# Performance work log

Measured on AMD Instinct MI355X. Metric: run time of the kernel, lower is better.

## Reference

```python
import jax, jax.numpy as jnp
import numpy as np

NUM_HEADS = 8
HEAD_DIM = 64
EMBED = NUM_HEADS * HEAD_DIM  # 512


def setup_inputs() -> dict:
    key = jax.random.key(0)
    ks = jax.random.split(key, 8)
    B, S = 4, 2048
    s = 1.0 / np.sqrt(HEAD_DIM)
    so = 1.0 / np.sqrt(EMBED)
    return {
        "queries": jax.random.normal(ks[0], (B, S, EMBED), jnp.float32),
        "keys": jax.random.normal(ks[1], (B, S, EMBED), jnp.float32),
        "values": jax.random.normal(ks[2], (B, S, EMBED), jnp.float32),
        "Wq": jax.random.uniform(ks[3], (HEAD_DIM, HEAD_DIM), jnp.float32, -s, s),
        "Wk": jax.random.uniform(ks[4], (HEAD_DIM, HEAD_DIM), jnp.float32, -s, s),
        "Wv": jax.random.uniform(ks[5], (HEAD_DIM, HEAD_DIM), jnp.float32, -s, s),
        "Wo": jax.random.uniform(ks[6], (EMBED, EMBED), jnp.float32, -so, so),
        "bo": jax.random.uniform(ks[7], (EMBED,), jnp.float32, -so, so),
    }


def reference(queries, keys, values, Wq, Wk, Wv, Wo, bo):
    B, Sq, _ = queries.shape
    # Faithful to source: keys/values are (buggily) reshaped from `queries`;
    # with equal seq lens this means k/v come from the queries tensor.
    q = queries.reshape(B, Sq, NUM_HEADS, HEAD_DIM)
    k = q
    v = q
    # per-head linear: torch Linear(x) = x @ W.T
    q = jnp.einsum('bshd,ed->bshe', q, Wq)
    k = jnp.einsum('bshd,ed->bshe', k, Wk)
    v = jnp.einsum('bshd,ed->bshe', v, Wv)
    sim = jnp.einsum('bqhd,bkhd->bhqk', q, k)  # [B,H,Sq,Sk]
    attn = jax.nn.softmax(sim * (1.0 / np.sqrt(HEAD_DIM)), axis=-1)
    out = jnp.einsum('bhqk,bkhd->bqhd', attn, v)
    out = out.reshape(B, Sq, EMBED)
    return out @ Wo.T + bo
```

## Files before the change

kernel.cpp:

```cpp
#include <hip/hip_runtime.h>
#include <cstddef>

#define S_ 2048
#define E_ 512
#define SPLIT_STRIDE 4194304u

typedef __attribute__((ext_vector_type(8)))  short bf16x8;
typedef __attribute__((ext_vector_type(16))) float f32x16;

__device__ __forceinline__ unsigned short f2bf(float f) {
    union { float f; unsigned u; } v; v.f = f;
    return (unsigned short)((v.u + 0x7FFFu + ((v.u >> 16) & 1u)) >> 16);
}
__device__ __forceinline__ unsigned pk2bf(float a, float b) {
    union { float f; unsigned u; } x, y; x.f = a; y.f = b;
    return __builtin_amdgcn_perm(y.u + 0x8000u, x.u + 0x8000u, 0x07060302u);
}
__device__ __forceinline__ float bflo(unsigned u) {
    union { unsigned u; float f; } v; v.u = u << 16; return v.f;
}
__device__ __forceinline__ float bfhi(unsigned u) {
    union { unsigned u; float f; } v; v.u = u & 0xffff0000u; return v.f;
}
__device__ __forceinline__ float fexp2(float x) {
    float r;
    asm("v_exp_f32 %0, %1" : "=v"(r) : "v"(x));
    return r;
}

__global__ __launch_bounds__(256) void prep_all(const float* __restrict__ X,
                                                const float* __restrict__ Wq,
                                                const float* __restrict__ Wk,
                                                const float* __restrict__ Wo,
                                                const float* __restrict__ Wv,
                                                unsigned short* __restrict__ Xbf,
                                                unsigned short* __restrict__ XTg,
                                                unsigned short* __restrict__ GT,
                                                unsigned short* __restrict__ W2) {
    __shared__ unsigned Tt[2320];
    const int bi = blockIdx.x, tid = threadIdx.x;
    if (bi < 1024) {
        const int st = bi & 31, h = (bi >> 5) & 7, b = bi >> 8;
        const int s0 = st * 64;
        const int j = tid >> 2, g = tid & 3;
        const float* src = X + ((size_t)(b * S_ + s0 + j) * E_) + h * 64 + g * 16;
        unsigned short us[16];
#pragma unroll
        for (int i = 0; i < 16; i += 4) {
            float4 f = *(const float4*)(src + i);
            us[i] = f2bf(f.x); us[i + 1] = f2bf(f.y);
            us[i + 2] = f2bf(f.z); us[i + 3] = f2bf(f.w);
        }
        size_t xb = ((size_t)(b * S_ + s0 + j) * E_) + h * 64 + g * 16;
        *(uint4*)&Xbf[xb]     = *(uint4*)&us[0];
        *(uint4*)&Xbf[xb + 8] = *(uint4*)&us[8];
        {
            const unsigned* p = (const unsigned*)us;
            const int base = (j >> 4) * 580 + (j & 15) * 36 + g * 8;
            *(uint4*)&Tt[base]     = *(const uint4*)&p[0];
            *(uint4*)&Tt[base + 4] = *(const uint4*)&p[4];
        }
        __syncthreads();
        const int d = tid >> 2;
        const int pm[16] = {0,1,2,3,8,9,10,11,4,5,6,7,12,13,14,15};
        const unsigned sel = (d & 1) ? 0x07060302u : 0x05040100u;
        const int rb = g * 580;
        const int d2 = d >> 1;
        unsigned o32[8];
#pragma unroll
        for (int k = 0; k < 8; ++k) {
            unsigned va = Tt[rb + pm[2 * k]     * 36 + d2];
            unsigned vb = Tt[rb + (pm[2 * k] + 1) * 36 + d2];
            o32[k] = __builtin_amdgcn_perm(vb, va, sel);
        }
        size_t tb = ((size_t)((b * 8 + h) * 64 + d)) * S_ + s0 + g * 16;
        *(uint4*)&XTg[tb]     = *(const uint4*)&o32[0];
        *(uint4*)&XTg[tb + 8] = *(const uint4*)&o32[4];
    } else if (bi < 1040) {
        int idx = (bi - 1024) * 256 + tid;
        int c = idx >> 6, d = idx & 63;
        float acc = 0.f;
#pragma unroll 8
        for (int e = 0; e < 64; ++e) acc += Wq[e * 64 + d] * Wk[e * 64 + c];
        GT[c * 64 + d] = f2bf(acc * 0.18033688011112042f);
    } else {
        int idx = (bi - 1040) * 256 + tid;
        int e = idx >> 9, f = idx & 511;
        int h = f >> 6, c = f & 63;
        const float* wo = Wo + e * 512 + h * 64;
        float acc = 0.f;
#pragma unroll 8
        for (int d = 0; d < 64; ++d) acc += wo[d] * Wv[d * 64 + c];
        W2[idx] = f2bf(acc);
    }
}

__global__ __launch_bounds__(128, 2) void attn_mfma(const unsigned short* __restrict__ Xbf,
                                                    const unsigned short* __restrict__ XTg,
                                                    const unsigned short* __restrict__ GT,
                                                    unsigned short* __restrict__ AOp,
                                                    float* __restrict__ Lp) {
    __shared__ union SM {
        unsigned short Q[128][72];
        unsigned char  cb[2][2][8192];
        unsigned short AOt[128][72];
    } sm;

    const int tid = threadIdx.x;
    const int w = tid >> 6, lane = tid & 63;
    const int lm = lane & 31, lh = lane >> 5;
    const int h = blockIdx.x & 7;
    const int rest = blockIdx.x >> 3;
    const int qt = rest & 15, b = (rest >> 4) & 3, split = rest >> 6;
    const int s0 = qt * 128, sk0 = split * (S_ / 2);

    {
        const int r = tid >> 1, c = (tid & 1) * 32;
#pragma unroll
        for (int p = 0; p < 2; ++p) {
            const unsigned short* src = Xbf + ((size_t)(b * S_ + s0 + 64 * p + r)) * E_ + h * 64 + c;
#pragma unroll
            for (int u = 0; u < 4; ++u)
                *(uint4*)&sm.Q[64 * p + r][c + u * 8] = *(const uint4*)(src + u * 8);
        }
    }
    __syncthreads();

    bf16x8 Ufrag[2][4];
    {
        f32x16 ua[2][2];
#pragma unroll
        for (int mt = 0; mt < 2; ++mt)
#pragma unroll
            for (int nt = 0; nt < 2; ++nt)
#pragma unroll
                for (int i = 0; i < 16; ++i) ua[mt][nt][i] = 0.f;
#pragma unroll
        for (int ks = 0; ks < 4; ++ks) {
            bf16x8 bG0 = *(const bf16x8*)&GT[(lm +  0) * 64 + ks * 16 + lh * 8];
            bf16x8 bG1 = *(const bf16x8*)&GT[(lm + 32) * 64 + ks * 16 + lh * 8];
#pragma unroll
            for (int mt = 0; mt < 2; ++mt) {
                bf16x8 aQ = *(const bf16x8*)&sm.Q[64 * w + 32 * mt + lm][ks * 16 + lh * 8];
                ua[mt][0] = __builtin_amdgcn_mfma_f32_32x32x16_bf16(aQ, bG0, ua[mt][0], 0, 0, 0);
                ua[mt][1] = __builtin_amdgcn_mfma_f32_32x32x16_bf16(aQ, bG1, ua[mt][1], 0, 0, 0);
            }
        }
#pragma unroll
        for (int mt = 0; mt < 2; ++mt)
#pragma unroll
            for (int nt = 0; nt < 2; ++nt)
#pragma unroll
                for (int r = 0; r < 16; ++r)
                    sm.Q[64 * w + 32 * mt + (r & 3) + 8 * (r >> 2) + 4 * lh][lm + 32 * nt] =
                        f2bf(ua[mt][nt][r]);
#pragma unroll
        for (int g = 0; g < 2; ++g)
#pragma unroll
            for (int ks = 0; ks < 4; ++ks)
                Ufrag[g][ks] = *(const bf16x8*)&sm.Q[64 * w + 32 * g + lm][ks * 16 + lh * 8];
    }
    __syncthreads();

    const int il = lane >> 3;
    const int swc = ((lane & 7) ^ (il & 7)) * 8;
    const unsigned short* gX0 = Xbf + ((size_t)(b * S_ + sk0 + 32 * w + il)) * E_ + h * 64 + swc;
    const unsigned short* gT0 = XTg + ((size_t)((b * 8 + h) * 64 + 32 * w + il)) * S_ + sk0 + swc;

#pragma unroll
    for (int i8 = 0; i8 < 4; ++i8) {
        __builtin_amdgcn_global_load_lds((const unsigned*)(gX0 + (size_t)i8 * 8 * E_),
                                         (unsigned*)&sm.cb[0][0][(4 * w + i8) * 1024], 16, 0, 0);
        __builtin_amdgcn_global_load_lds((const unsigned*)(gT0 + (size_t)i8 * 8 * S_),
                                         (unsigned*)&sm.cb[0][1][(4 * w + i8) * 1024], 16, 0, 0);
    }
    __syncthreads();

    float lsum0 = 0.f, lsum1 = 0.f;
    f32x16 AO[2][2];
#pragma unroll
    for (int mt = 0; mt < 2; ++mt)
#pragma unroll
        for (int nt = 0; nt < 2; ++nt)
#pragma unroll
            for (int i = 0; i < 16; ++i) AO[mt][nt][i] = 0.f;

    f32x16 zv;
#pragma unroll
    for (int i = 0; i < 16; ++i) zv[i] = 0.f;

    const int xorr = (lm & 7) << 4;

    for (int ck = 0; ck < 16; ++ck) {
        const int rb = ck & 1;
        if (ck < 15) {
            const unsigned short* sX = gX0 + (size_t)(ck + 1) * 64 * E_;
            const unsigned short* sT = gT0 + (ck + 1) * 64;
            unsigned char* dX = &sm.cb[rb ^ 1][0][4 * w * 1024];
            unsigned char* dT = &sm.cb[rb ^ 1][1][4 * w * 1024];
#pragma unroll
            for (int i8 = 0; i8 < 4; ++i8) {
                __builtin_amdgcn_global_load_lds((const unsigned*)(sX + (size_t)i8 * 8 * E_),
                                                 (unsigned*)(dX + i8 * 1024), 16, 0, 0);
                __builtin_amdgcn_global_load_lds((const unsigned*)(sT + (size_t)i8 * 8 * S_),
                                                 (unsigned*)(dT + i8 * 1024), 16, 0, 0);
            }
        }

        const unsigned char* bX = sm.cb[rb][0];
        const unsigned char* bT = sm.cb[rb][1];

        f32x16 sc[2][2];
        __builtin_amdgcn_s_setprio(1);
#pragma unroll
        for (int mt = 0; mt < 2; ++mt) {
            bf16x8 aX = *(const bf16x8*)(bX + (32 * mt + lm) * 128 + ((lh * 16) ^ xorr));
            sc[mt][0] = __builtin_amdgcn_mfma_f32_32x32x16_bf16(aX, Ufrag[0][0], zv, 0, 0, 0);
            sc[mt][1] = __builtin_amdgcn_mfma_f32_32x32x16_bf16(aX, Ufrag[1][0], zv, 0, 0, 0);
        }
#pragma unroll
        for (int ks = 1; ks < 4; ++ks)
#pragma unroll
            for (int mt = 0; mt < 2; ++mt) {
                bf16x8 aX = *(const bf16x8*)(bX + (32 * mt + lm) * 128 + ((ks * 32 + lh * 16) ^ xorr));
                sc[mt][0] = __builtin_amdgcn_mfma_f32_32x32x16_bf16(aX, Ufrag[0][ks], sc[mt][0], 0, 0, 0);
                sc[mt][1] = __builtin_amdgcn_mfma_f32_32x32x16_bf16(aX, Ufrag[1][ks], sc[mt][1], 0, 0, 0);
            }
        __builtin_amdgcn_s_setprio(0);

#pragma unroll
        for (int js = 0; js < 4; ++js) {
            const int mt = js >> 1, jh = js & 1;
            union { unsigned u[4]; bf16x8 v; } bP0, bP1;
#pragma unroll
            for (int i = 0; i < 4; ++i) {
                const int qq = 2 * jh + (i >> 1);
                float pa = fexp2(sc[mt][0][qq * 4 + 2 * (i & 1)]);
                float pb = fexp2(sc[mt][0][qq * 4 + 2 * (i & 1) + 1]);
                lsum0 += pa + pb;
                bP0.u[i] = pk2bf(pa, pb);
                float pc = fexp2(sc[mt][1][qq * 4 + 2 * (i & 1)]);
                float pd = fexp2(sc[mt][1][qq * 4 + 2 * (i & 1) + 1]);
                lsum1 += pc + pd;
                bP1.u[i] = pk2bf(pc, pd);
            }
            __builtin_amdgcn_s_setprio(1);
#pragma unroll
            for (int mtv = 0; mtv < 2; ++mtv) {
                bf16x8 aT = *(const bf16x8*)(bT + (32 * mtv + lm) * 128 + ((js * 32 + lh * 16) ^ xorr));
                AO[mtv][0] = __builtin_amdgcn_mfma_f32_32x32x16_bf16(aT, bP0.v, AO[mtv][0], 0, 0, 0);
                AO[mtv][1] = __builtin_amdgcn_mfma_f32_32x32x16_bf16(aT, bP1.v, AO[mtv][1], 0, 0, 0);
            }
            __builtin_amdgcn_s_setprio(0);
        }
        __syncthreads();
    }

    lsum0 += __shfl_xor(lsum0, 32);
    lsum1 += __shfl_xor(lsum1, 32);
#pragma unroll
    for (int mtv = 0; mtv < 2; ++mtv)
#pragma unroll
        for (int nt = 0; nt < 2; ++nt)
#pragma unroll
            for (int qq = 0; qq < 4; ++qq) {
                const int d0 = 32 * mtv + 8 * qq + 4 * lh;
                const int row = 64 * w + 32 * nt + lm;
                *(unsigned*)&sm.AOt[row][d0] =
                    pk2bf(AO[mtv][nt][qq * 4 + 0], AO[mtv][nt][qq * 4 + 1]);
                *(unsigned*)&sm.AOt[row][d0 + 2] =
                    pk2bf(AO[mtv][nt][qq * 4 + 2], AO[mtv][nt][qq * 4 + 3]);
            }
    __syncthreads();
    {
        const int r = tid >> 1, c = (tid & 1) * 32;
#pragma unroll
        for (int p = 0; p < 2; ++p) {
            unsigned short* dst = AOp + (size_t)split * SPLIT_STRIDE
                                + ((size_t)(b * S_ + s0 + 64 * p + r)) * E_ + h * 64 + c;
#pragma unroll
            for (int u = 0; u < 4; ++u)
                *(uint4*)(dst + u * 8) = *(const uint4*)&sm.AOt[64 * p + r][c + u * 8];
        }
    }
    if (lane < 32) {
        const size_t lb = ((size_t)(split * 4 + b) * 8 + h) * S_ + s0 + 64 * w;
        Lp[lb + lm]      = lsum0;
        Lp[lb + 32 + lm] = lsum1;
    }
}

__global__ __launch_bounds__(256) void out_gemm_bf(const unsigned short* __restrict__ AOp,
                                                   const float* __restrict__ Lp,
                                                   const unsigned short* __restrict__ W2,
                                                   const float* __restrict__ bo,
                                                   float* __restrict__ out) {
    __shared__ unsigned short At[64][72];
    __shared__ unsigned short Bt[64][72];
    const int tid = threadIdx.x;
    const int w = tid >> 6, lane = tid & 63;
    const int lm = lane & 31, lh = lane >> 5;
    const int et = blockIdx.x >> 7;
    const int rt = (blockIdx.x & 7) * 16 + ((blockIdx.x >> 3) & 15);
    const int r0 = rt * 64, e0 = et * 64;
    const int rr = tid >> 2, cc = (tid & 3) * 16;
    const int srow = r0 + rr, bb = srow >> 11, ss = srow & 2047;

    f32x16 acc;
#pragma unroll
    for (int i = 0; i < 16; ++i) acc[i] = 0.f;

    for (int k0 = 0; k0 < 512; k0 += 64) {
        const int hh = k0 >> 6;
        const float linv = 1.0f / (Lp[((size_t)(bb)*8 + hh) * S_ + ss] +
                                   Lp[((size_t)(4 + bb) * 8 + hh) * S_ + ss]);
        __syncthreads();
        {
            const unsigned short* a0 = AOp + (size_t)srow * 512 + k0 + cc;
            const unsigned short* a1 = a0 + SPLIT_STRIDE;
            uint4 u0 = *(const uint4*)a0, u0b = *(const uint4*)(a0 + 8);
            uint4 u1 = *(const uint4*)a1, u1b = *(const uint4*)(a1 + 8);
            uint4 o, ob;
            o.x  = pk2bf((bflo(u0.x) + bflo(u1.x)) * linv, (bfhi(u0.x) + bfhi(u1.x)) * linv);
            o.y  = pk2bf((bflo(u0.y) + bflo(u1.y)) * linv, (bfhi(u0.y) + bfhi(u1.y)) * linv);
            o.z  = pk2bf((bflo(u0.z) + bflo(u1.z)) * linv, (bfhi(u0.z) + bfhi(u1.z)) * linv);
            o.w  = pk2bf((bflo(u0.w) + bflo(u1.w)) * linv, (bfhi(u0.w) + bfhi(u1.w)) * linv);
            ob.x = pk2bf((bflo(u0b.x) + bflo(u1b.x)) * linv, (bfhi(u0b.x) + bfhi(u1b.x)) * linv);
            ob.y = pk2bf((bflo(u0b.y) + bflo(u1b.y)) * linv, (bfhi(u0b.y) + bfhi(u1b.y)) * linv);
            ob.z = pk2bf((bflo(u0b.z) + bflo(u1b.z)) * linv, (bfhi(u0b.z) + bfhi(u1b.z)) * linv);
            ob.w = pk2bf((bflo(u0b.w) + bflo(u1b.w)) * linv, (bfhi(u0b.w) + bfhi(u1b.w)) * linv);
            *(uint4*)&At[rr][cc]     = o;
            *(uint4*)&At[rr][cc + 8] = ob;
            const unsigned short* sb = W2 + (size_t)(e0 + rr) * 512 + k0 + cc;
            *(uint4*)&Bt[rr][cc]     = *(const uint4*)sb;
            *(uint4*)&Bt[rr][cc + 8] = *(const uint4*)(sb + 8);
        }
        __syncthreads();
#pragma unroll
        for (int ks = 0; ks < 4; ++ks) {
            bf16x8 aA = *(const bf16x8*)&At[32 * (w & 1) + lm][ks * 16 + lh * 8];
            bf16x8 bW = *(const bf16x8*)&Bt[32 * (w >> 1) + lm][ks * 16 + lh * 8];
            acc = __builtin_amdgcn_mfma_f32_32x32x16_bf16(aA, bW, acc, 0, 0, 0);
        }
    }
    const float bv = bo[e0 + 32 * (w >> 1) + lm];
#pragma unroll
    for (int r = 0; r < 16; ++r) {
        int orow = r0 + 32 * (w & 1) + (r & 3) + 8 * (r >> 2) + 4 * lh;
        out[(size_t)orow * 512 + e0 + 32 * (w >> 1) + lm] = acc[r] + bv;
    }
}

extern "C" void kernel_launch(void* const* d_in, const int* in_sizes, int n_in,
                              void* d_out, int out_size, void* d_ws, size_t ws_size,
                              hipStream_t stream) {
    (void)in_sizes; (void)n_in; (void)out_size; (void)ws_size;
    const float* X  = (const float*)d_in[0];
    const float* Wq = (const float*)d_in[3];
    const float* Wk = (const float*)d_in[4];
    const float* Wv = (const float*)d_in[5];
    const float* Wo = (const float*)d_in[6];
    const float* bo = (const float*)d_in[7];

    float* ws = (float*)d_ws;
    unsigned short* W2bf = (unsigned short*)ws;
    unsigned short* GT   = (unsigned short*)(ws + 131072);
    unsigned short* Xbf  = (unsigned short*)(ws + 133120);
    unsigned short* XTg  = (unsigned short*)(ws + 2230272);
    unsigned short* AOp  = (unsigned short*)(ws + 4327424);
    float*          Lp   = ws + 8521728;

    prep_all   <<<2064, 256, 0, stream>>>(X, Wq, Wk, Wo, Wv, Xbf, XTg, GT, W2bf);
    attn_mfma  <<<1024, 128, 0, stream>>>(Xbf, XTg, GT, AOp, Lp);
    out_gemm_bf<<<1024, 256, 0, stream>>>(AOp, Lp, W2bf, bo, (float*)d_out);
}
```

Baseline: 161.1 us.

## Split attention key range four ways with smaller KV chunks

Templates the attention and output GEMM kernels on the number of key splits. When the workspace is large enough it launches 2048 attention blocks, each covering a quarter of the keys, and the output GEMM sums four partial outputs and row sums. KV chunks shrink from 64 to 32 keys, which halves the LDS buffers and allows a launch bound of 4 blocks per SM for more parallelism and occupancy. The cost is more partial-output traffic and reduction work in the output GEMM, plus more loop iterations and barriers per key.

```diff
diff --git a/kernel.cpp b/kernel.cpp
--- a/kernel.cpp
+++ b/kernel.cpp
@@ -95,14 +95,17 @@
     }
 }
 
-__global__ __launch_bounds__(128, 2) void attn_mfma(const unsigned short* __restrict__ Xbf,
+template<int NSPLIT>
+__global__ __launch_bounds__(128, 4) void attn_mfma(const unsigned short* __restrict__ Xbf,
                                                     const unsigned short* __restrict__ XTg,
                                                     const unsigned short* __restrict__ GT,
                                                     unsigned short* __restrict__ AOp,
                                                     float* __restrict__ Lp) {
+    constexpr int KPB = S_ / NSPLIT;
+    constexpr int CHUNKS = KPB / 32;
     __shared__ union SM {
         unsigned short Q[128][72];
-        unsigned char  cb[2][2][8192];
+        unsigned char  cb[2][2][4096];
         unsigned short AOt[128][72];
     } sm;
 
@@ -112,7 +115,7 @@
     const int h = blockIdx.x & 7;
     const int rest = blockIdx.x >> 3;
     const int qt = rest & 15, b = (rest >> 4) & 3, split = rest >> 6;
-    const int s0 = qt * 128, sk0 = split * (S_ / 2);
+    const int s0 = qt * 128, sk0 = split * KPB;
 
     {
         const int r = tid >> 1, c = (tid & 1) * 32;
@@ -162,47 +165,50 @@
     }
     __syncthreads();
 
-    const int il = lane >> 3;
-    const int swc = ((lane & 7) ^ (il & 7)) * 8;
-    const unsigned short* gX0 = Xbf + ((size_t)(b * S_ + sk0 + 32 * w + il)) * E_ + h * 64 + swc;
-    const unsigned short* gT0 = XTg + ((size_t)((b * 8 + h) * 64 + 32 * w + il)) * S_ + sk0 + swc;
-
-#pragma unroll
-    for (int i8 = 0; i8 < 4; ++i8) {
+    const unsigned short* gX0 = Xbf
+        + ((size_t)(b * S_ + sk0 + 16 * w + (lane >> 3))) * E_ + h * 64
+        + ((lane & 7) ^ (lane >> 3)) * 8;
+    const unsigned short* gT0 = XTg
+        + ((size_t)((b * 8 + h) * 64 + 32 * w + (lane >> 2))) * S_ + sk0
+        + ((lane & 3) ^ ((lane >> 2) & 3)) * 8;
+
+#pragma unroll
+    for (int i8 = 0; i8 < 2; ++i8) {
         __builtin_amdgcn_global_load_lds((const unsigned*)(gX0 + (size_t)i8 * 8 * E_),
-                                         (unsigned*)&sm.cb[0][0][(4 * w + i8) * 1024], 16, 0, 0);
-        __builtin_amdgcn_global_load_lds((const unsigned*)(gT0 + (size_t)i8 * 8 * S_),
-                                         (unsigned*)&sm.cb[0][1][(4 * w + i8) * 1024], 16, 0, 0);
+                                         (unsigned*)&sm.cb[0][0][w * 2048 + i8 * 1024], 16, 0, 0);
+        __builtin_amdgcn_global_load_lds((const unsigned*)(gT0 + (size_t)i8 * 16 * S_),
+                                         (unsigned*)&sm.cb[0][1][w * 2048 + i8 * 1024], 16, 0, 0);
     }
     __syncthreads();
 
     float lsum0 = 0.f, lsum1 = 0.f;
     f32x16 AO[2][2];
 #pragma unroll
-    for (int mt = 0; mt < 2; ++mt)
-#pragma unroll
-        for (int nt = 0; nt < 2; ++nt)
-#pragma unroll
-            for (int i = 0; i < 16; ++i) AO[mt][nt][i] = 0.f;
+    for (int mtv = 0; mtv < 2; ++mtv)
+#pragma unroll
+        for (int g = 0; g < 2; ++g)
+#pragma unroll
+            for (int i = 0; i < 16; ++i) AO[mtv][g][i] = 0.f;
 
     f32x16 zv;
 #pragma unroll
     for (int i = 0; i < 16; ++i) zv[i] = 0.f;
 
-    const int xorr = (lm & 7) << 4;
-
-    for (int ck = 0; ck < 16; ++ck) {
+    const int xorrX = (lm & 7) << 4;
+    const int xorrT = (lm & 3) << 4;
+
+    for (int ck = 0; ck < CHUNKS; ++ck) {
         const int rb = ck & 1;
-        if (ck < 15) {
-            const unsigned short* sX = gX0 + (size_t)(ck + 1) * 64 * E_;
-            const unsigned short* sT = gT0 + (ck + 1) * 64;
-            unsigned char* dX = &sm.cb[rb ^ 1][0][4 * w * 1024];
-            unsigned char* dT = &sm.cb[rb ^ 1][1][4 * w * 1024];
-#pragma unroll
-            for (int i8 = 0; i8 < 4; ++i8) {
+        if (ck < CHUNKS - 1) {
+            const unsigned short* sX = gX0 + (size_t)(ck + 1) * 32 * E_;
+            const unsigned short* sT = gT0 + (ck + 1) * 32;
+            unsigned char* dX = &sm.cb[rb ^ 1][0][w * 2048];
+            unsigned char* dT = &sm.cb[rb ^ 1][1][w * 2048];
+#pragma unroll
+            for (int i8 = 0; i8 < 2; ++i8) {
                 __builtin_amdgcn_global_load_lds((const unsigned*)(sX + (size_t)i8 * 8 * E_),
                                                  (unsigned*)(dX + i8 * 1024), 16, 0, 0);
-                __builtin_amdgcn_global_load_lds((const unsigned*)(sT + (size_t)i8 * 8 * S_),
+                __builtin_amdgcn_global_load_lds((const unsigned*)(sT + (size_t)i8 * 16 * S_),
                                                  (unsigned*)(dT + i8 * 1024), 16, 0, 0);
             }
         }
@@ -210,44 +216,40 @@
         const unsigned char* bX = sm.cb[rb][0];
         const unsigned char* bT = sm.cb[rb][1];
 
-        f32x16 sc[2][2];
+        f32x16 sc[2];
         __builtin_amdgcn_s_setprio(1);
-#pragma unroll
-        for (int mt = 0; mt < 2; ++mt) {
-            bf16x8 aX = *(const bf16x8*)(bX + (32 * mt + lm) * 128 + ((lh * 16) ^ xorr));
-            sc[mt][0] = __builtin_amdgcn_mfma_f32_32x32x16_bf16(aX, Ufrag[0][0], zv, 0, 0, 0);
-            sc[mt][1] = __builtin_amdgcn_mfma_f32_32x32x16_bf16(aX, Ufrag[1][0], zv, 0, 0, 0);
-        }
-#pragma unroll
-        for (int ks = 1; ks < 4; ++ks)
-#pragma unroll
-            for (int mt = 0; mt < 2; ++mt) {
-                bf16x8 aX = *(const bf16x8*)(bX + (32 * mt + lm) * 128 + ((ks * 32 + lh * 16) ^ xorr));
-                sc[mt][0] = __builtin_amdgcn_mfma_f32_32x32x16_bf16(aX, Ufrag[0][ks], sc[mt][0], 0, 0, 0);
-                sc[mt][1] = __builtin_amdgcn_mfma_f32_32x32x16_bf16(aX, Ufrag[1][ks], sc[mt][1], 0, 0, 0);
-            }
+        {
+            bf16x8 aX = *(const bf16x8*)(bX + lm * 128 + ((lh * 16) ^ xorrX));
+            sc[0] = __builtin_amdgcn_mfma_f32_32x32x16_bf16(aX, Ufrag[0][0], zv, 0, 0, 0);
+            sc[1] = __builtin_amdgcn_mfma_f32_32x32x16_bf16(aX, Ufrag[1][0], zv, 0, 0, 0);
+        }
+#pragma unroll
+        for (int ks = 1; ks < 4; ++ks) {
+            bf16x8 aX = *(const bf16x8*)(bX + lm * 128 + ((ks * 32 + lh * 16) ^ xorrX));
+            sc[0] = __builtin_amdgcn_mfma_f32_32x32x16_bf16(aX, Ufrag[0][ks], sc[0], 0, 0, 0);
+            sc[1] = __builtin_amdgcn_mfma_f32_32x32x16_bf16(aX, Ufrag[1][ks], sc[1], 0, 0, 0);
+        }
         __builtin_amdgcn_s_setprio(0);
 
 #pragma unroll
-        for (int js = 0; js < 4; ++js) {
-            const int mt = js >> 1, jh = js & 1;
+        for (int s = 0; s < 2; ++s) {
             union { unsigned u[4]; bf16x8 v; } bP0, bP1;
 #pragma unroll
             for (int i = 0; i < 4; ++i) {
-                const int qq = 2 * jh + (i >> 1);
-                float pa = fexp2(sc[mt][0][qq * 4 + 2 * (i & 1)]);
-                float pb = fexp2(sc[mt][0][qq * 4 + 2 * (i & 1) + 1]);
+                const int ra = 8 * s + 4 * (i >> 1) + 2 * (i & 1);
+                float pa = fexp2(sc[0][ra]);
+                float pb = fexp2(sc[0][ra + 1]);
                 lsum0 += pa + pb;
                 bP0.u[i] = pk2bf(pa, pb);
-                float pc = fexp2(sc[mt][1][qq * 4 + 2 * (i & 1)]);
-                float pd = fexp2(sc[mt][1][qq * 4 + 2 * (i & 1) + 1]);
+                float pc = fexp2(sc[1][ra]);
+                float pd = fexp2(sc[1][ra + 1]);
                 lsum1 += pc + pd;
                 bP1.u[i] = pk2bf(pc, pd);
             }
             __builtin_amdgcn_s_setprio(1);
 #pragma unroll
             for (int mtv = 0; mtv < 2; ++mtv) {
-                bf16x8 aT = *(const bf16x8*)(bT + (32 * mtv + lm) * 128 + ((js * 32 + lh * 16) ^ xorr));
+                bf16x8 aT = *(const bf16x8*)(bT + (32 * mtv + lm) * 64 + ((s * 32 + lh * 16) ^ xorrT));
                 AO[mtv][0] = __builtin_amdgcn_mfma_f32_32x32x16_bf16(aT, bP0.v, AO[mtv][0], 0, 0, 0);
                 AO[mtv][1] = __builtin_amdgcn_mfma_f32_32x32x16_bf16(aT, bP1.v, AO[mtv][1], 0, 0, 0);
             }
@@ -290,6 +292,7 @@
     }
 }
 
+template<int NSPLIT>
 __global__ __launch_bounds__(256) void out_gemm_bf(const unsigned short* __restrict__ AOp,
                                                    const float* __restrict__ Lp,
                                                    const unsigned short* __restrict__ W2,
@@ -312,23 +315,39 @@
 
     for (int k0 = 0; k0 < 512; k0 += 64) {
         const int hh = k0 >> 6;
-        const float linv = 1.0f / (Lp[((size_t)(bb)*8 + hh) * S_ + ss] +
-                                   Lp[((size_t)(4 + bb) * 8 + hh) * S_ + ss]);
+        float lt = 0.f;
+#pragma unroll
+        for (int sp = 0; sp < NSPLIT; ++sp)
+            lt += Lp[((size_t)(sp * 4 + bb) * 8 + hh) * S_ + ss];
+        const float linv = 1.0f / lt;
         __syncthreads();
         {
             const unsigned short* a0 = AOp + (size_t)srow * 512 + k0 + cc;
-            const unsigned short* a1 = a0 + SPLIT_STRIDE;
-            uint4 u0 = *(const uint4*)a0, u0b = *(const uint4*)(a0 + 8);
-            uint4 u1 = *(const uint4*)a1, u1b = *(const uint4*)(a1 + 8);
+            float fa[16];
+#pragma unroll
+            for (int i = 0; i < 16; ++i) fa[i] = 0.f;
+#pragma unroll
+            for (int sp = 0; sp < NSPLIT; ++sp) {
+                const unsigned short* ap = a0 + (size_t)sp * SPLIT_STRIDE;
+                uint4 ua = *(const uint4*)ap, ub = *(const uint4*)(ap + 8);
+                const unsigned* pu = (const unsigned*)&ua;
+                const unsigned* pv = (const unsigned*)&ub;
+#pragma unroll
+                for (int k = 0; k < 4; ++k) {
+                    fa[2 * k]     += bflo(pu[k]);
+                    fa[2 * k + 1] += bfhi(pu[k]);
+                    fa[8 + 2 * k]     += bflo(pv[k]);
+                    fa[8 + 2 * k + 1] += bfhi(pv[k]);
+                }
+            }
             uint4 o, ob;
-            o.x  = pk2bf((bflo(u0.x) + bflo(u1.x)) * linv, (bfhi(u0.x) + bfhi(u1.x)) * linv);
-            o.y  = pk2bf((bflo(u0.y) + bflo(u1.y)) * linv, (bfhi(u0.y) + bfhi(u1.y)) * linv);
-            o.z  = pk2bf((bflo(u0.z) + bflo(u1.z)) * linv, (bfhi(u0.z) + bfhi(u1.z)) * linv);
-            o.w  = pk2bf((bflo(u0.w) + bflo(u1.w)) * linv, (bfhi(u0.w) + bfhi(u1.w)) * linv);
-            ob.x = pk2bf((bflo(u0b.x) + bflo(u1b.x)) * linv, (bfhi(u0b.x) + bfhi(u1b.x)) * linv);
-            ob.y = pk2bf((bflo(u0b.y) + bflo(u1b.y)) * linv, (bfhi(u0b.y) + bfhi(u1b.y)) * linv);
-            ob.z = pk2bf((bflo(u0b.z) + bflo(u1b.z)) * linv, (bfhi(u0b.z) + bfhi(u1b.z)) * linv);
-            ob.w = pk2bf((bflo(u0b.w) + bflo(u1b.w)) * linv, (bfhi(u0b.w) + bfhi(u1b.w)) * linv);
+            unsigned* po  = (unsigned*)&o;
+            unsigned* pob = (unsigned*)&ob;
+#pragma unroll
+            for (int k = 0; k < 4; ++k) {
+                po[k]  = pk2bf(fa[2 * k] * linv, fa[2 * k + 1] * linv);
+                pob[k] = pk2bf(fa[8 + 2 * k] * linv, fa[8 + 2 * k + 1] * linv);
+            }
             *(uint4*)&At[rr][cc]     = o;
             *(uint4*)&At[rr][cc + 8] = ob;
             const unsigned short* sb = W2 + (size_t)(e0 + rr) * 512 + k0 + cc;
@@ -354,7 +373,7 @@
 extern "C" void kernel_launch(void* const* d_in, const int* in_sizes, int n_in,
                               void* d_out, int out_size, void* d_ws, size_t ws_size,
                               hipStream_t stream) {
-    (void)in_sizes; (void)n_in; (void)out_size; (void)ws_size;
+    (void)in_sizes; (void)n_in; (void)out_size;
     const float* X  = (const float*)d_in[0];
     const float* Wq = (const float*)d_in[3];
     const float* Wk = (const float*)d_in[4];
@@ -368,9 +387,17 @@
     unsigned short* Xbf  = (unsigned short*)(ws + 133120);
     unsigned short* XTg  = (unsigned short*)(ws + 2230272);
     unsigned short* AOp  = (unsigned short*)(ws + 4327424);
-    float*          Lp   = ws + 8521728;
-
-    prep_all   <<<2064, 256, 0, stream>>>(X, Wq, Wk, Wo, Wv, Xbf, XTg, GT, W2bf);
-    attn_mfma  <<<1024, 128, 0, stream>>>(Xbf, XTg, GT, AOp, Lp);
-    out_gemm_bf<<<1024, 256, 0, stream>>>(AOp, Lp, W2bf, bo, (float*)d_out);
-}
+
+    prep_all<<<2064, 256, 0, stream>>>(X, Wq, Wk, Wo, Wv, Xbf, XTg, GT, W2bf);
+
+    const size_t need4 = (size_t)(12716032 + 262144) * 4;
+    if (ws_size >= need4) {
+        float* Lp = ws + 12716032;
+        attn_mfma<4><<<2048, 128, 0, stream>>>(Xbf, XTg, GT, AOp, Lp);
+        out_gemm_bf<4><<<1024, 256, 0, stream>>>(AOp, Lp, W2bf, bo, (float*)d_out);
+    } else {
+        float* Lp = ws + 8521728;
+        attn_mfma<2><<<1024, 128, 0, stream>>>(Xbf, XTg, GT, AOp, Lp);
+        out_gemm_bf<2><<<1024, 256, 0, stream>>>(AOp, Lp, W2bf, bo, (float*)d_out);
+    }
+}
```

New measurement: 227.3 us. 1.41x slower.

## Load K/V MFMA fragments directly from global memory instead of LDS staging

Applied to the files above, without the earlier changes.

Removes the double-buffered LDS staging of K and V tiles, which used async global_load_lds and a barrier per chunk. Each wave now reads its MFMA operand fragments straight from global memory (relying on L1/L2 caches), which drops per-iteration __syncthreads and shrinks shared memory to allow more residency. The trade-off is uncoalesced 16-byte global reads, duplicated across the two waves in a block, with no prefetch overlap, so load latency sits directly on the MFMA path.

```diff
diff --git a/kernel.cpp b/kernel.cpp
--- a/kernel.cpp
+++ b/kernel.cpp
@@ -102,7 +102,6 @@
                                                     float* __restrict__ Lp) {
     __shared__ union SM {
         unsigned short Q[128][72];
-        unsigned char  cb[2][2][8192];
         unsigned short AOt[128][72];
     } sm;
 
@@ -160,21 +159,9 @@
             for (int ks = 0; ks < 4; ++ks)
                 Ufrag[g][ks] = *(const bf16x8*)&sm.Q[64 * w + 32 * g + lm][ks * 16 + lh * 8];
     }
-    __syncthreads();
-
-    const int il = lane >> 3;
-    const int swc = ((lane & 7) ^ (il & 7)) * 8;
-    const unsigned short* gX0 = Xbf + ((size_t)(b * S_ + sk0 + 32 * w + il)) * E_ + h * 64 + swc;
-    const unsigned short* gT0 = XTg + ((size_t)((b * 8 + h) * 64 + 32 * w + il)) * S_ + sk0 + swc;
-
-#pragma unroll
-    for (int i8 = 0; i8 < 4; ++i8) {
-        __builtin_amdgcn_global_load_lds((const unsigned*)(gX0 + (size_t)i8 * 8 * E_),
-                                         (unsigned*)&sm.cb[0][0][(4 * w + i8) * 1024], 16, 0, 0);
-        __builtin_amdgcn_global_load_lds((const unsigned*)(gT0 + (size_t)i8 * 8 * S_),
-                                         (unsigned*)&sm.cb[0][1][(4 * w + i8) * 1024], 16, 0, 0);
-    }
-    __syncthreads();
+
+    const unsigned short* kb  = Xbf + ((size_t)(b * S_ + sk0 + lm)) * E_ + h * 64 + lh * 8;
+    const unsigned short* vb_ = XTg + ((size_t)((b * 8 + h) * 64 + lm)) * S_ + sk0 + lh * 8;
 
     float lsum0 = 0.f, lsum1 = 0.f;
     f32x16 AO[2][2];
@@ -189,32 +176,14 @@
 #pragma unroll
     for (int i = 0; i < 16; ++i) zv[i] = 0.f;
 
-    const int xorr = (lm & 7) << 4;
-
     for (int ck = 0; ck < 16; ++ck) {
-        const int rb = ck & 1;
-        if (ck < 15) {
-            const unsigned short* sX = gX0 + (size_t)(ck + 1) * 64 * E_;
-            const unsigned short* sT = gT0 + (ck + 1) * 64;
-            unsigned char* dX = &sm.cb[rb ^ 1][0][4 * w * 1024];
-            unsigned char* dT = &sm.cb[rb ^ 1][1][4 * w * 1024];
-#pragma unroll
-            for (int i8 = 0; i8 < 4; ++i8) {
-                __builtin_amdgcn_global_load_lds((const unsigned*)(sX + (size_t)i8 * 8 * E_),
-                                                 (unsigned*)(dX + i8 * 1024), 16, 0, 0);
-                __builtin_amdgcn_global_load_lds((const unsigned*)(sT + (size_t)i8 * 8 * S_),
-                                                 (unsigned*)(dT + i8 * 1024), 16, 0, 0);
-            }
-        }
-
-        const unsigned char* bX = sm.cb[rb][0];
-        const unsigned char* bT = sm.cb[rb][1];
+        const unsigned short* kc = kb + (size_t)(ck * 64) * E_;
 
         f32x16 sc[2][2];
         __builtin_amdgcn_s_setprio(1);
 #pragma unroll
         for (int mt = 0; mt < 2; ++mt) {
-            bf16x8 aX = *(const bf16x8*)(bX + (32 * mt + lm) * 128 + ((lh * 16) ^ xorr));
+            bf16x8 aX = *(const bf16x8*)(kc + (size_t)(32 * mt) * E_);
             sc[mt][0] = __builtin_amdgcn_mfma_f32_32x32x16_bf16(aX, Ufrag[0][0], zv, 0, 0, 0);
             sc[mt][1] = __builtin_amdgcn_mfma_f32_32x32x16_bf16(aX, Ufrag[1][0], zv, 0, 0, 0);
         }
@@ -222,7 +191,7 @@
         for (int ks = 1; ks < 4; ++ks)
 #pragma unroll
             for (int mt = 0; mt < 2; ++mt) {
-                bf16x8 aX = *(const bf16x8*)(bX + (32 * mt + lm) * 128 + ((ks * 32 + lh * 16) ^ xorr));
+                bf16x8 aX = *(const bf16x8*)(kc + (size_t)(32 * mt) * E_ + ks * 16);
                 sc[mt][0] = __builtin_amdgcn_mfma_f32_32x32x16_bf16(aX, Ufrag[0][ks], sc[mt][0], 0, 0, 0);
                 sc[mt][1] = __builtin_amdgcn_mfma_f32_32x32x16_bf16(aX, Ufrag[1][ks], sc[mt][1], 0, 0, 0);
             }
@@ -247,15 +216,15 @@
             __builtin_amdgcn_s_setprio(1);
 #pragma unroll
             for (int mtv = 0; mtv < 2; ++mtv) {
-                bf16x8 aT = *(const bf16x8*)(bT + (32 * mtv + lm) * 128 + ((js * 32 + lh * 16) ^ xorr));
+                bf16x8 aT = *(const bf16x8*)(vb_ + (size_t)(32 * mtv) * S_ + ck * 64 + js * 16);
                 AO[mtv][0] = __builtin_amdgcn_mfma_f32_32x32x16_bf16(aT, bP0.v, AO[mtv][0], 0, 0, 0);
                 AO[mtv][1] = __builtin_amdgcn_mfma_f32_32x32x16_bf16(aT, bP1.v, AO[mtv][1], 0, 0, 0);
             }
             __builtin_amdgcn_s_setprio(0);
         }
-        __syncthreads();
-    }
-
+    }
+
+    __syncthreads();
     lsum0 += __shfl_xor(lsum0, 32);
     lsum1 += __shfl_xor(lsum1, 32);
 #pragma unroll
```

Measured after the change: 186.1 us. 15.5% more time.
